# Optimization experiments

Measured on AMD Instinct MI355X. Metric: run time of the kernel, lower is better.

The kernel has to match this reference:

```python
import jax, jax.numpy as jnp
import numpy as np

H = 1024   # hidden_size
V = 32000  # output_size (vocab)
S = 4096   # encoder seq_len
L = 1      # n_layers


def setup_inputs() -> dict:
    key = jax.random.key(0)
    ks = jax.random.split(key, 12)
    scale = 0.02
    return {
        "word_input": jax.random.randint(ks[0], (1,), 0, V),
        "last_hidden": jax.random.normal(ks[1], (L, 1, H), jnp.float32),
        "encoder_hiddens": jax.random.normal(ks[2], (S, 1, H), jnp.float32),
        "embedding": jax.random.normal(ks[3], (V, H), jnp.float32) * scale,
        "w_ih": jax.random.normal(ks[4], (3 * H, H), jnp.float32) * scale,
        "w_hh": jax.random.normal(ks[5], (3 * H, H), jnp.float32) * scale,
        "b_ih": jax.random.normal(ks[6], (3 * H,), jnp.float32) * scale,
        "b_hh": jax.random.normal(ks[7], (3 * H,), jnp.float32) * scale,
        "attn_w": jax.random.normal(ks[8], (H, H), jnp.float32) * scale,
        "attn_b": jax.random.normal(ks[9], (H,), jnp.float32) * scale,
        "out_w": jax.random.normal(ks[10], (V, 2 * H), jnp.float32) * scale,
        "out_b": jax.random.normal(ks[11], (V,), jnp.float32) * scale,
    }


def reference(word_input, last_hidden, encoder_hiddens, embedding,
              w_ih, w_hh, b_ih, b_hh, attn_w, attn_b, out_w, out_b):
    h_dim = embedding.shape[1]
    # embedding lookup -> GRU single step (PyTorch GRU cell math)
    x = embedding[word_input[0]]            # [H]
    h0 = last_hidden[0, 0]                  # [H]
    gx = w_ih @ x + b_ih                    # [3H]
    gh = w_hh @ h0 + b_hh                   # [3H]
    r = jax.nn.sigmoid(gx[:h_dim] + gh[:h_dim])
    z = jax.nn.sigmoid(gx[h_dim:2 * h_dim] + gh[h_dim:2 * h_dim])
    n = jnp.tanh(gx[2 * h_dim:] + r * gh[2 * h_dim:])
    h = (1.0 - z) * n + z * h0              # rnn_output / new hidden [H]
    # Bahdanau-style scores: dot(hidden, attn(enc_i)) for all i, batched
    enc = encoder_hiddens[:, 0, :]          # [S, H]
    scores = (enc @ attn_w.T + attn_b) @ h  # [S]
    attn = jax.nn.softmax(scores)           # [S]
    context = attn @ enc                    # [H]
    output = jnp.concatenate([h, context]) @ out_w.T + out_b  # [V]
    return (output[None, :], h[None, None, :], attn[None, None, :])
```

## Files before the change

### kernel.cpp

```cpp
#include <hip/hip_runtime.h>
#include <cstddef>

#define Hn 1024
#define Vn 32000
#define Sn 4096

__device__ __forceinline__ float wave_reduce_sum(float v) {
#pragma unroll
    for (int o = 32; o > 0; o >>= 1) v += __shfl_down(v, o, 64);
    return v;
}
__device__ __forceinline__ float wave_reduce_max(float v) {
#pragma unroll
    for (int o = 32; o > 0; o >>= 1) v = fmaxf(v, __shfl_down(v, o, 64));
    return v;
}


__global__ __launch_bounds__(256) void k_gru(const int* __restrict__ word,
                                             const float* __restrict__ emb,
                                             const float* __restrict__ h0,
                                             const float* __restrict__ w_ih,
                                             const float* __restrict__ w_hh,
                                             const float* __restrict__ b_ih,
                                             const float* __restrict__ b_hh,
                                             float* __restrict__ ws_h,
                                             float* __restrict__ ws_ctx,
                                             float* __restrict__ out_h)
{
    const int k = blockIdx.x;
    const int t = threadIdx.x;

    if (k == 0) {
#pragma unroll
        for (int i = 0; i < 4; ++i) ws_ctx[t + i * 256] = 0.f;
    }

    const float* x = emb + (size_t)word[0] * Hn;
    const float4 xv = ((const float4*)x)[t];
    const float4 hv = ((const float4*)h0)[t];

    float acc[6];
    const float* rows[6] = {
        w_ih + (size_t)k * Hn, w_ih + (size_t)(k + Hn) * Hn, w_ih + (size_t)(k + 2 * Hn) * Hn,
        w_hh + (size_t)k * Hn, w_hh + (size_t)(k + Hn) * Hn, w_hh + (size_t)(k + 2 * Hn) * Hn
    };
#pragma unroll
    for (int g = 0; g < 6; ++g) {
        const float4 w = ((const float4*)rows[g])[t];
        const float4 vv = (g < 3) ? xv : hv;
        acc[g] = w.x * vv.x + w.y * vv.y + w.z * vv.z + w.w * vv.w;
    }

    __shared__ float red[6][4];
    const int wv = t >> 6, lane = t & 63;
#pragma unroll
    for (int g = 0; g < 6; ++g) {
        const float s = wave_reduce_sum(acc[g]);
        if (lane == 0) red[g][wv] = s;
    }
    __syncthreads();
    if (t == 0) {
        float g0 = red[0][0] + red[0][1] + red[0][2] + red[0][3] + b_ih[k];
        float g1 = red[1][0] + red[1][1] + red[1][2] + red[1][3] + b_ih[k + Hn];
        float g2 = red[2][0] + red[2][1] + red[2][2] + red[2][3] + b_ih[k + 2 * Hn];
        float g3 = red[3][0] + red[3][1] + red[3][2] + red[3][3] + b_hh[k];
        float g4 = red[4][0] + red[4][1] + red[4][2] + red[4][3] + b_hh[k + Hn];
        float g5 = red[5][0] + red[5][1] + red[5][2] + red[5][3] + b_hh[k + 2 * Hn];
        float r = 1.f / (1.f + expf(-(g0 + g3)));
        float z = 1.f / (1.f + expf(-(g1 + g4)));
        float n = tanhf(g2 + r * g5);
        float hk = (1.f - z) * n + z * h0[k];
        ws_h[k]  = hk;
        out_h[k] = hk;
    }
}

__global__ __launch_bounds__(256) void k_attnv(const float* __restrict__ attn_w,
                                               const float* __restrict__ ws_h,
                                               float* __restrict__ v)
{
    const int t = threadIdx.x;
    const int tj = t >> 4;
    const int tk = t & 15;
    const int k = blockIdx.x * 16 + tk;
    float acc = 0.f;
    for (int j = tj; j < Hn; j += 16)
        acc += attn_w[(size_t)j * Hn + k] * ws_h[j];
    __shared__ float p[16][17];
    p[tj][tk] = acc;
    __syncthreads();
    if (t < 16) {
        float s = 0.f;
#pragma unroll
        for (int j = 0; j < 16; ++j) s += p[j][t];
        v[blockIdx.x * 16 + t] = s;
    }
}

__global__ __launch_bounds__(256) void k_scores(const float* __restrict__ enc,
                                                const float* __restrict__ ws_v,
                                                float* __restrict__ scores)
{
    __shared__ float v[Hn];
    const int t = threadIdx.x;
    ((float4*)v)[t] = ((const float4*)ws_v)[t];
    __syncthreads();
    const int wv = t >> 6, lane = t & 63;
    const int s = blockIdx.x * 4 + wv;
    const float* row = enc + (size_t)s * Hn;
    float acc = 0.f;
#pragma unroll
    for (int k = 0; k < 4; ++k) {
        const int idx = k * 256 + lane * 4;
        const float4 e = *(const float4*)(row + idx);
        acc += e.x * v[idx] + e.y * v[idx + 1] + e.z * v[idx + 2] + e.w * v[idx + 3];
    }
    acc = wave_reduce_sum(acc);
    if (lane == 0) scores[s] = acc;
}

__global__ __launch_bounds__(256) void k_ctx(const float* __restrict__ enc,
                                             const float* __restrict__ scores,
                                             float* __restrict__ ctx,
                                             float* __restrict__ out_attn)
{
    const int t = threadIdx.x, bid = blockIdx.x;
    const int wv = t >> 6, lane = t & 63;
    __shared__ float red[4];
    __shared__ float aw[64];

    float4 sc[4];
#pragma unroll
    for (int i = 0; i < 4; ++i) sc[i] = ((const float4*)scores)[i * 256 + t];
    float m = -1e30f;
#pragma unroll
    for (int i = 0; i < 4; ++i)
        m = fmaxf(m, fmaxf(fmaxf(sc[i].x, sc[i].y), fmaxf(sc[i].z, sc[i].w)));
    m = wave_reduce_max(m);
    if (lane == 0) red[wv] = m;
    __syncthreads();
    const float mx = fmaxf(fmaxf(red[0], red[1]), fmaxf(red[2], red[3]));
    float ps = 0.f;
#pragma unroll
    for (int i = 0; i < 4; ++i)
        ps += expf(sc[i].x - mx) + expf(sc[i].y - mx) + expf(sc[i].z - mx) + expf(sc[i].w - mx);
    ps = wave_reduce_sum(ps);
    __syncthreads();
    if (lane == 0) red[wv] = ps;
    __syncthreads();
    const float inv = 1.f / (red[0] + red[1] + red[2] + red[3]);

    const int s0 = bid * 64;
    if (t < 64) {
        const float a = expf(scores[s0 + t] - mx) * inv;
        aw[t] = a;
        out_attn[s0 + t] = a;
    }
    __syncthreads();

    float acc0 = 0.f, acc1 = 0.f, acc2 = 0.f, acc3 = 0.f;
    const float* base = enc + (size_t)s0 * Hn;
#pragma unroll 4
    for (int s = 0; s < 64; ++s) {
        const float a = aw[s];
        const float* row = base + (size_t)s * Hn;
        acc0 += a * row[t];
        acc1 += a * row[t + 256];
        acc2 += a * row[t + 512];
        acc3 += a * row[t + 768];
    }
    atomicAdd(&ctx[t],       acc0);
    atomicAdd(&ctx[t + 256], acc1);
    atomicAdd(&ctx[t + 512], acc2);
    atomicAdd(&ctx[t + 768], acc3);
}

__global__ __launch_bounds__(256) void k_out(const float* __restrict__ out_w,
                                             const float* __restrict__ out_b,
                                             const float* __restrict__ c2,
                                             float* __restrict__ out)
{
    __shared__ float c[2 * Hn];
    const int t = threadIdx.x;
    ((float4*)c)[t]       = ((const float4*)c2)[t];
    ((float4*)c)[t + 256] = ((const float4*)c2)[t + 256];
    __syncthreads();
    const int wv = t >> 6, lane = t & 63;
    const int row = blockIdx.x * 4 + wv;
    const float* w = out_w + (size_t)row * (2 * Hn);
    float acc = 0.f;
#pragma unroll
    for (int k = 0; k < 8; ++k) {
        const int idx = k * 256 + lane * 4;
        const float4 w4 = *(const float4*)(w + idx);
        acc += w4.x * c[idx] + w4.y * c[idx + 1] + w4.z * c[idx + 2] + w4.w * c[idx + 3];
    }
    acc = wave_reduce_sum(acc);
    if (lane == 0) out[row] = acc + out_b[row];
}

extern "C" void kernel_launch(void* const* d_in, const int* in_sizes, int n_in,
                              void* d_out, int out_size, void* d_ws, size_t ws_size,
                              hipStream_t stream) {
    const int*   word   = (const int*)d_in[0];
    const float* h_last = (const float*)d_in[1];
    const float* enc    = (const float*)d_in[2];
    const float* emb    = (const float*)d_in[3];
    const float* w_ih   = (const float*)d_in[4];
    const float* w_hh   = (const float*)d_in[5];
    const float* b_ih   = (const float*)d_in[6];
    const float* b_hh   = (const float*)d_in[7];
    const float* attn_w = (const float*)d_in[8];
    const float* out_w  = (const float*)d_in[10];
    const float* out_b  = (const float*)d_in[11];
    float* out = (float*)d_out;
    float* ws  = (float*)d_ws;

    float* ws_h      = ws;
    float* ws_ctx    = ws + 1024;
    float* ws_v      = ws + 2048;
    float* ws_scores = ws + 3072;

    k_gru<<<Hn, 256, 0, stream>>>(word, emb, h_last, w_ih, w_hh, b_ih, b_hh, ws_h, ws_ctx, out + Vn);
    k_attnv<<<Hn / 16, 256, 0, stream>>>(attn_w, ws_h, ws_v);
    k_scores<<<Sn / 4, 256, 0, stream>>>(enc, ws_v, ws_scores);
    k_ctx<<<Sn / 64, 256, 0, stream>>>(enc, ws_scores, ws_ctx, out + Vn + Hn);
    k_out<<<Vn / 4, 256, 0, stream>>>(out_w, out_b, ws, out);
}
```

Baseline: 86.19 us.

## Split output projection and overlap h-half with attention kernels

Splits the output projection into an h-dependent half and a context-dependent half. The h-half rows are spread across the attention kernels as extra blocks, so their reads of out_w overlap with the small, latency-bound attention stages. A final kernel adds the context half into the output. This hides part of the out_w streaming behind underutilized kernels, at the cost of an extra read-modify-write of the output and more complex block dispatch.

After: 83.98 us. 2.6% less time.

```diff
diff --git a/kernel.cpp b/kernel.cpp
--- a/kernel.cpp
+++ b/kernel.cpp
@@ -16,6 +16,29 @@
     return v;
 }
 
+
+__device__ __forceinline__ void out_h_rows(const float* __restrict__ out_w,
+                                           const float* __restrict__ out_b,
+                                           const float* __restrict__ ws_h,
+                                           float* __restrict__ out,
+                                           int row_base, int t)
+{
+    __shared__ float c[Hn];
+    ((float4*)c)[t] = ((const float4*)ws_h)[t];
+    __syncthreads();
+    const int wv = t >> 6, lane = t & 63;
+    const int row = row_base + wv;
+    const float* w = out_w + (size_t)row * (2 * Hn);
+    float acc = 0.f;
+#pragma unroll
+    for (int k = 0; k < 4; ++k) {
+        const int idx = k * 256 + lane * 4;
+        const float4 w4 = *(const float4*)(w + idx);
+        acc += w4.x * c[idx] + w4.y * c[idx + 1] + w4.z * c[idx + 2] + w4.w * c[idx + 3];
+    }
+    acc = wave_reduce_sum(acc);
+    if (lane == 0) out[row] = acc + out_b[row];
+}
 
 __global__ __launch_bounds__(256) void k_gru(const int* __restrict__ word,
                                              const float* __restrict__ emb,
@@ -76,128 +99,148 @@
     }
 }
 
-__global__ __launch_bounds__(256) void k_attnv(const float* __restrict__ attn_w,
-                                               const float* __restrict__ ws_h,
-                                               float* __restrict__ v)
-{
+__global__ __launch_bounds__(256) void k_a(const float* __restrict__ attn_w,
+                                           const float* __restrict__ ws_h,
+                                           float* __restrict__ v,
+                                           const float* __restrict__ out_w,
+                                           const float* __restrict__ out_b,
+                                           float* __restrict__ out)
+{
+    const int t = threadIdx.x, bid = blockIdx.x;
+    if (bid < 64) {
+        const int tj = t >> 4, tk = t & 15;
+        const int k = bid * 16 + tk;
+        float acc = 0.f;
+        for (int j = tj; j < Hn; j += 16)
+            acc += attn_w[(size_t)j * Hn + k] * ws_h[j];
+        __shared__ float p[16][17];
+        p[tj][tk] = acc;
+        __syncthreads();
+        if (t < 16) {
+            float s = 0.f;
+#pragma unroll
+            for (int j = 0; j < 16; ++j) s += p[j][t];
+            v[bid * 16 + t] = s;
+        }
+    } else {
+        out_h_rows(out_w, out_b, ws_h, out, (bid - 64) * 4, t);
+    }
+}
+
+__global__ __launch_bounds__(256) void k_b(const float* __restrict__ enc,
+                                           const float* __restrict__ ws_v,
+                                           float* __restrict__ scores,
+                                           const float* __restrict__ ws_h,
+                                           const float* __restrict__ out_w,
+                                           const float* __restrict__ out_b,
+                                           float* __restrict__ out)
+{
+    const int t = threadIdx.x, bid = blockIdx.x;
+    if (bid < 1024) {
+        __shared__ float vsm[Hn];
+        ((float4*)vsm)[t] = ((const float4*)ws_v)[t];
+        __syncthreads();
+        const int wv = t >> 6, lane = t & 63;
+        const int s = bid * 4 + wv;
+        const float* row = enc + (size_t)s * Hn;
+        float acc = 0.f;
+#pragma unroll
+        for (int k = 0; k < 4; ++k) {
+            const int idx = k * 256 + lane * 4;
+            const float4 e = *(const float4*)(row + idx);
+            acc += e.x * vsm[idx] + e.y * vsm[idx + 1] + e.z * vsm[idx + 2] + e.w * vsm[idx + 3];
+        }
+        acc = wave_reduce_sum(acc);
+        if (lane == 0) scores[s] = acc;
+    } else {
+        out_h_rows(out_w, out_b, ws_h, out, 10668 + (bid - 1024) * 4, t);
+    }
+}
+
+__global__ __launch_bounds__(256) void k_c(const float* __restrict__ enc,
+                                           const float* __restrict__ scores,
+                                           float* __restrict__ ctx,
+                                           float* __restrict__ out_attn,
+                                           const float* __restrict__ ws_h,
+                                           const float* __restrict__ out_w,
+                                           const float* __restrict__ out_b,
+                                           float* __restrict__ out)
+{
+    const int t = threadIdx.x, bid = blockIdx.x;
+    if (bid < 64) {
+        const int wv = t >> 6, lane = t & 63;
+        __shared__ float red[4];
+        __shared__ float aw[64];
+
+        float4 sc[4];
+#pragma unroll
+        for (int i = 0; i < 4; ++i) sc[i] = ((const float4*)scores)[i * 256 + t];
+        float m = -1e30f;
+#pragma unroll
+        for (int i = 0; i < 4; ++i)
+            m = fmaxf(m, fmaxf(fmaxf(sc[i].x, sc[i].y), fmaxf(sc[i].z, sc[i].w)));
+        m = wave_reduce_max(m);
+        if (lane == 0) red[wv] = m;
+        __syncthreads();
+        const float mx = fmaxf(fmaxf(red[0], red[1]), fmaxf(red[2], red[3]));
+        float ps = 0.f;
+#pragma unroll
+        for (int i = 0; i < 4; ++i)
+            ps += expf(sc[i].x - mx) + expf(sc[i].y - mx) + expf(sc[i].z - mx) + expf(sc[i].w - mx);
+        ps = wave_reduce_sum(ps);
+        __syncthreads();
+        if (lane == 0) red[wv] = ps;
+        __syncthreads();
+        const float inv = 1.f / (red[0] + red[1] + red[2] + red[3]);
+
+        const int s0 = bid * 64;
+        if (t < 64) {
+            const float a = expf(scores[s0 + t] - mx) * inv;
+            aw[t] = a;
+            out_attn[s0 + t] = a;
+        }
+        __syncthreads();
+
+        float acc0 = 0.f, acc1 = 0.f, acc2 = 0.f, acc3 = 0.f;
+        const float* base = enc + (size_t)s0 * Hn;
+#pragma unroll 4
+        for (int s = 0; s < 64; ++s) {
+            const float a = aw[s];
+            const float* row = base + (size_t)s * Hn;
+            acc0 += a * row[t];
+            acc1 += a * row[t + 256];
+            acc2 += a * row[t + 512];
+            acc3 += a * row[t + 768];
+        }
+        atomicAdd(&ctx[t],       acc0);
+        atomicAdd(&ctx[t + 256], acc1);
+        atomicAdd(&ctx[t + 512], acc2);
+        atomicAdd(&ctx[t + 768], acc3);
+    } else {
+        out_h_rows(out_w, out_b, ws_h, out, 21336 + (bid - 64) * 4, t);
+    }
+}
+
+__global__ __launch_bounds__(256) void k_out_ctx(const float* __restrict__ out_w,
+                                                 const float* __restrict__ ws_ctx,
+                                                 float* __restrict__ out)
+{
+    __shared__ float c[Hn];
     const int t = threadIdx.x;
-    const int tj = t >> 4;
-    const int tk = t & 15;
-    const int k = blockIdx.x * 16 + tk;
-    float acc = 0.f;
-    for (int j = tj; j < Hn; j += 16)
-        acc += attn_w[(size_t)j * Hn + k] * ws_h[j];
-    __shared__ float p[16][17];
-    p[tj][tk] = acc;
-    __syncthreads();
-    if (t < 16) {
-        float s = 0.f;
-#pragma unroll
-        for (int j = 0; j < 16; ++j) s += p[j][t];
-        v[blockIdx.x * 16 + t] = s;
-    }
-}
-
-__global__ __launch_bounds__(256) void k_scores(const float* __restrict__ enc,
-                                                const float* __restrict__ ws_v,
-                                                float* __restrict__ scores)
-{
-    __shared__ float v[Hn];
-    const int t = threadIdx.x;
-    ((float4*)v)[t] = ((const float4*)ws_v)[t];
-    __syncthreads();
-    const int wv = t >> 6, lane = t & 63;
-    const int s = blockIdx.x * 4 + wv;
-    const float* row = enc + (size_t)s * Hn;
-    float acc = 0.f;
-#pragma unroll
-    for (int k = 0; k < 4; ++k) {
-        const int idx = k * 256 + lane * 4;
-        const float4 e = *(const float4*)(row + idx);
-        acc += e.x * v[idx] + e.y * v[idx + 1] + e.z * v[idx + 2] + e.w * v[idx + 3];
-    }
-    acc = wave_reduce_sum(acc);
-    if (lane == 0) scores[s] = acc;
-}
-
-__global__ __launch_bounds__(256) void k_ctx(const float* __restrict__ enc,
-                                             const float* __restrict__ scores,
-                                             float* __restrict__ ctx,
-                                             float* __restrict__ out_attn)
-{
-    const int t = threadIdx.x, bid = blockIdx.x;
-    const int wv = t >> 6, lane = t & 63;
-    __shared__ float red[4];
-    __shared__ float aw[64];
-
-    float4 sc[4];
-#pragma unroll
-    for (int i = 0; i < 4; ++i) sc[i] = ((const float4*)scores)[i * 256 + t];
-    float m = -1e30f;
-#pragma unroll
-    for (int i = 0; i < 4; ++i)
-        m = fmaxf(m, fmaxf(fmaxf(sc[i].x, sc[i].y), fmaxf(sc[i].z, sc[i].w)));
-    m = wave_reduce_max(m);
-    if (lane == 0) red[wv] = m;
-    __syncthreads();
-    const float mx = fmaxf(fmaxf(red[0], red[1]), fmaxf(red[2], red[3]));
-    float ps = 0.f;
-#pragma unroll
-    for (int i = 0; i < 4; ++i)
-        ps += expf(sc[i].x - mx) + expf(sc[i].y - mx) + expf(sc[i].z - mx) + expf(sc[i].w - mx);
-    ps = wave_reduce_sum(ps);
-    __syncthreads();
-    if (lane == 0) red[wv] = ps;
-    __syncthreads();
-    const float inv = 1.f / (red[0] + red[1] + red[2] + red[3]);
-
-    const int s0 = bid * 64;
-    if (t < 64) {
-        const float a = expf(scores[s0 + t] - mx) * inv;
-        aw[t] = a;
-        out_attn[s0 + t] = a;
-    }
-    __syncthreads();
-
-    float acc0 = 0.f, acc1 = 0.f, acc2 = 0.f, acc3 = 0.f;
-    const float* base = enc + (size_t)s0 * Hn;
-#pragma unroll 4
-    for (int s = 0; s < 64; ++s) {
-        const float a = aw[s];
-        const float* row = base + (size_t)s * Hn;
-        acc0 += a * row[t];
-        acc1 += a * row[t + 256];
-        acc2 += a * row[t + 512];
-        acc3 += a * row[t + 768];
-    }
-    atomicAdd(&ctx[t],       acc0);
-    atomicAdd(&ctx[t + 256], acc1);
-    atomicAdd(&ctx[t + 512], acc2);
-    atomicAdd(&ctx[t + 768], acc3);
-}
-
-__global__ __launch_bounds__(256) void k_out(const float* __restrict__ out_w,
-                                             const float* __restrict__ out_b,
-                                             const float* __restrict__ c2,
-                                             float* __restrict__ out)
-{
-    __shared__ float c[2 * Hn];
-    const int t = threadIdx.x;
-    ((float4*)c)[t]       = ((const float4*)c2)[t];
-    ((float4*)c)[t + 256] = ((const float4*)c2)[t + 256];
+    ((float4*)c)[t] = ((const float4*)ws_ctx)[t];
     __syncthreads();
     const int wv = t >> 6, lane = t & 63;
     const int row = blockIdx.x * 4 + wv;
-    const float* w = out_w + (size_t)row * (2 * Hn);
+    const float* w = out_w + (size_t)row * (2 * Hn) + Hn;
     float acc = 0.f;
 #pragma unroll
-    for (int k = 0; k < 8; ++k) {
+    for (int k = 0; k < 4; ++k) {
         const int idx = k * 256 + lane * 4;
         const float4 w4 = *(const float4*)(w + idx);
         acc += w4.x * c[idx] + w4.y * c[idx + 1] + w4.z * c[idx + 2] + w4.w * c[idx + 3];
     }
     acc = wave_reduce_sum(acc);
-    if (lane == 0) out[row] = acc + out_b[row];
+    if (lane == 0) out[row] += acc;
 }
 
 extern "C" void kernel_launch(void* const* d_in, const int* in_sizes, int n_in,
@@ -223,8 +266,8 @@
     float* ws_scores = ws + 3072;
 
     k_gru<<<Hn, 256, 0, stream>>>(word, emb, h_last, w_ih, w_hh, b_ih, b_hh, ws_h, ws_ctx, out + Vn);
-    k_attnv<<<Hn / 16, 256, 0, stream>>>(attn_w, ws_h, ws_v);
-    k_scores<<<Sn / 4, 256, 0, stream>>>(enc, ws_v, ws_scores);
-    k_ctx<<<Sn / 64, 256, 0, stream>>>(enc, ws_scores, ws_ctx, out + Vn + Hn);
-    k_out<<<Vn / 4, 256, 0, stream>>>(out_w, out_b, ws, out);
-}
+    k_a<<<64 + 2667, 256, 0, stream>>>(attn_w, ws_h, ws_v, out_w, out_b, out);
+    k_b<<<1024 + 2667, 256, 0, stream>>>(enc, ws_v, ws_scores, ws_h, out_w, out_b, out);
+    k_c<<<64 + 2666, 256, 0, stream>>>(enc, ws_scores, ws_ctx, out + Vn + Hn, ws_h, out_w, out_b, out);
+    k_out_ctx<<<Vn / 4, 256, 0, stream>>>(out_w, ws_ctx, out);
+}
```
